# Performance work log

Hardware: AMD Instinct MI355X
Metric: run time of the kernel (lower is better)

The kernel has to match this reference:

```python
import jax, jax.numpy as jnp
import numpy as np
from jax import lax

B, T, S, H, E, V = 32, 64, 64, 512, 512, 32000


def setup_inputs() -> dict:
    key = jax.random.key(0)
    ks = jax.random.split(key, 10)
    s = 0.02
    return {
        "sequence": jax.random.randint(ks[0], (B, T), 0, V),
        "encoder_outputs": jax.random.normal(ks[1], (S, B, H), jnp.float32),
        "encoder_hidden": jax.random.normal(ks[2], (B, H), jnp.float32),
        "encoder_cell": jax.random.normal(ks[3], (B, H), jnp.float32),
        "embedding": jax.random.normal(ks[4], (V, E), jnp.float32) * s,
        "W_ih": jax.random.normal(ks[5], (4 * H, E + H), jnp.float32) * s,
        "b_ih": jnp.zeros((4 * H,), jnp.float32),
        "W_hh": jax.random.normal(ks[6], (4 * H, H), jnp.float32) * s,
        "b_hh": jnp.zeros((4 * H,), jnp.float32),
        "W_in_proj": jax.random.normal(ks[7], (H, H), jnp.float32) * s,
        "b_in_proj": jnp.zeros((H,), jnp.float32),
        "W_out_proj": jax.random.normal(ks[8], (H, 2 * H), jnp.float32) * s,
        "b_out_proj": jnp.zeros((H,), jnp.float32),
        "W_final": jax.random.normal(ks[9], (V, H), jnp.float32) * s,
        "b_final": jnp.zeros((V,), jnp.float32),
    }


def reference(sequence, encoder_outputs, encoder_hidden, encoder_cell,
              embedding, W_ih, b_ih, W_hh, b_hh,
              W_in_proj, b_in_proj, W_out_proj, b_out_proj,
              W_final, b_final):
    # embed: [B,T,E] -> [T,B,E] (dropout_in = 0 -> identity)
    x = embedding[sequence].transpose(1, 0, 2)
    input_feed = jnp.zeros((B, H), x.dtype)

    def step(carry, x_t):
        h, c, feed = carry
        inp = jnp.concatenate([x_t, feed], axis=1)          # [B, E+H]
        gates = inp @ W_ih.T + b_ih + h @ W_hh.T + b_hh     # [B, 4H]
        i, f, g, o = jnp.split(gates, 4, axis=1)
        c = jax.nn.sigmoid(f) * c + jax.nn.sigmoid(i) * jnp.tanh(g)
        h = jax.nn.sigmoid(o) * jnp.tanh(c)
        # attention layer (scores computed but unused downstream, as in source)
        xp = h @ W_in_proj.T + b_in_proj                    # [B, H]
        scores = jax.nn.softmax(
            jnp.einsum('sbh,bh->sb', encoder_outputs, xp), axis=0)  # [S, B]
        out = jnp.tanh(jnp.concatenate([xp, h], axis=1) @ W_out_proj.T + b_out_proj)
        return (h, c, out), (out, scores)

    _, (outs, _attn) = lax.scan(step, (encoder_hidden, encoder_cell, input_feed), x)
    # outs: [T,B,H] -> [B,T,H] -> logits [B,T,V]
    logits = outs.transpose(1, 0, 2) @ W_final.T + b_final
    return logits
```

## Files before the change

### kernel.cpp

```cpp
#include <hip/hip_runtime.h>
#include <hip/hip_bf16.h>

#define BB 32
#define TT 64
#define HH 512
#define EE 512
#define VV 32000

typedef float f32x4 __attribute__((ext_vector_type(4)));
typedef float f32x16 __attribute__((ext_vector_type(16)));
typedef __bf16 bf16x8 __attribute__((ext_vector_type(8)));
typedef unsigned short u16x8 __attribute__((ext_vector_type(8)));

static __device__ __forceinline__ unsigned short f2bf(float f) {
  unsigned int u = __builtin_bit_cast(unsigned int, f);
  u += 0x7fffu + ((u >> 16) & 1u);
  return (unsigned short)(u >> 16);
}

static __device__ __forceinline__ void gload16(const void* g, void* l) {
  __builtin_amdgcn_global_load_lds(
      (const __attribute__((address_space(1))) void*)g,
      (__attribute__((address_space(3))) void*)l, 16, 0, 0);
}

__global__ __launch_bounds__(256) void k_cvt_bf16(const float* __restrict__ in,
                                                  unsigned short* __restrict__ out,
                                                  int n8) {
  int tid = blockIdx.x * 256 + threadIdx.x;
  if (tid >= n8) return;
  int idx = tid * 8;
  float4 a = *(const float4*)(in + idx);
  float4 b = *(const float4*)(in + idx + 4);
  u16x8 o;
  o[0] = f2bf(a.x); o[1] = f2bf(a.y); o[2] = f2bf(a.z); o[3] = f2bf(a.w);
  o[4] = f2bf(b.x); o[5] = f2bf(b.y); o[6] = f2bf(b.z); o[7] = f2bf(b.w);
  *(u16x8*)(out + idx) = o;
}

__global__ __launch_bounds__(256) void k_trcvt(const float* __restrict__ in,
                                               unsigned short* __restrict__ out) {
  __shared__ float tile[32][33];
  const int tx = threadIdx.x & 31, ty = threadIdx.x >> 5;
  const int k0 = blockIdx.x * 32, m0 = blockIdx.y * 32;
#pragma unroll
  for (int r = 0; r < 4; ++r)
    tile[ty + r * 8][tx] = in[(size_t)(k0 + ty + r * 8) * 512 + m0 + tx];
  __syncthreads();
#pragma unroll
  for (int r = 0; r < 4; ++r)
    out[(size_t)(m0 + ty + r * 8) * 512 + k0 + tx] = f2bf(tile[tx][ty + r * 8]);
}

__global__ __launch_bounds__(256) void k_emb(const int* __restrict__ seq,
                                             const float* __restrict__ emb,
                                             unsigned short* __restrict__ out) {
  int tid = blockIdx.x * 256 + threadIdx.x;
  int idx = tid * 8;
  int m = idx >> 9;
  int e0 = idx & 511;
  int t = m >> 5, b = m & 31;
  int s = seq[b * TT + t];
  const float* src = emb + (size_t)s * EE + e0;
  float4 a = *(const float4*)(src);
  float4 c = *(const float4*)(src + 4);
  u16x8 o;
  o[0] = f2bf(a.x); o[1] = f2bf(a.y); o[2] = f2bf(a.z); o[3] = f2bf(a.w);
  o[4] = f2bf(c.x); o[5] = f2bf(c.y); o[6] = f2bf(c.z); o[7] = f2bf(c.w);
  *(u16x8*)(out + m * EE + e0) = o;
}

__global__ __launch_bounds__(256) void k_beff(const float* __restrict__ W_out,
                                              const float* __restrict__ b_in,
                                              const float* __restrict__ b_out,
                                              float* __restrict__ b_eff) {
  int i = blockIdx.x * 256 + threadIdx.x;
  if (i >= HH) return;
  float acc = b_out[i];
  for (int k = 0; k < HH; ++k) acc += W_out[i * 1024 + k] * b_in[k];
  b_eff[i] = acc;
}

__global__ __launch_bounds__(256) void k_gemm(const unsigned short* __restrict__ A, int lda,
                                              const unsigned short* __restrict__ Bm, int ldb,
                                              float* __restrict__ C, int ldc,
                                              const float* __restrict__ bias1,
                                              const float* __restrict__ bias2,
                                              const float* __restrict__ biasR1,
                                              const float* __restrict__ biasR2,
                                              const float* __restrict__ Cadd, int ldadd,
                                              int K, int m_panels) {
  __shared__ unsigned short As[128 * 32];
  __shared__ unsigned short Bs[128 * 32];
  const int tx = threadIdx.x;
  const int lane = tx & 63, w = tx >> 6;
  const int wrow = (w >> 1) * 64, wcol = (w & 1) * 64;
  const int l15 = lane & 15, lk = lane >> 4;
  const int nb = gridDim.x;
  const int swz = (blockIdx.x & 7) * (nb >> 3) + (blockIdx.x >> 3);
  const int m0 = (swz % m_panels) * 128, n0 = (swz / m_panels) * 128;
  const int r_lane = lane >> 2;
  const int k_lane = (lane & 3) * 8;
  f32x4 acc[4][4] = {};
  for (int k0 = 0; k0 < K; k0 += 32) {
#pragma unroll
    for (int h = 0; h < 2; ++h) {
      int r0 = w * 32 + h * 16;
      gload16(A + (size_t)(m0 + r0 + r_lane) * lda + k0 + k_lane, &As[r0 * 32]);
      gload16(Bm + (size_t)(n0 + r0 + r_lane) * ldb + k0 + k_lane, &Bs[r0 * 32]);
    }
    asm volatile("s_waitcnt vmcnt(0)" ::: "memory");
    __syncthreads();
    bf16x8 av[4], bv[4];
#pragma unroll
    for (int mi = 0; mi < 4; ++mi)
      av[mi] = __builtin_bit_cast(bf16x8, *(const int4*)(&As[(wrow + mi * 16 + l15) * 32 + lk * 8]));
#pragma unroll
    for (int ni = 0; ni < 4; ++ni)
      bv[ni] = __builtin_bit_cast(bf16x8, *(const int4*)(&Bs[(wcol + ni * 16 + l15) * 32 + lk * 8]));
#pragma unroll
    for (int mi = 0; mi < 4; ++mi)
#pragma unroll
      for (int ni = 0; ni < 4; ++ni)
        acc[mi][ni] = __builtin_amdgcn_mfma_f32_16x16x32_bf16(av[mi], bv[ni], acc[mi][ni], 0, 0, 0);
    __syncthreads();
  }
#pragma unroll
  for (int mi = 0; mi < 4; ++mi) {
#pragma unroll
    for (int ni = 0; ni < 4; ++ni) {
      int row = m0 + wrow + mi * 16 + lk * 4;
      int col = n0 + wcol + ni * 16 + l15;
      float bb = 0.f;
      if (bias1) bb += bias1[col];
      if (bias2) bb += bias2[col];
#pragma unroll
      for (int q = 0; q < 4; ++q) {
        float bR = 0.f;
        if (biasR1) bR += biasR1[row + q];
        if (biasR2) bR += biasR2[row + q];
        float ad = Cadd ? Cadd[(size_t)(row + q) * ldadd + col] : 0.f;
        C[(size_t)(row + q) * ldc + col] = acc[mi][ni][q] + bb + bR + ad;
      }
    }
  }
}

static __device__ __forceinline__ void gbar(unsigned* __restrict__ bar, unsigned gen) {
  __syncthreads();
  if (threadIdx.x == 0) {
    asm volatile("s_waitcnt vmcnt(0)" ::: "memory");
    __hip_atomic_store(&bar[blockIdx.x], gen, __ATOMIC_RELAXED, __HIP_MEMORY_SCOPE_AGENT);
  }
  if (threadIdx.x < 64) {
    while (__hip_atomic_load(&bar[threadIdx.x], __ATOMIC_RELAXED, __HIP_MEMORY_SCOPE_AGENT) < gen) {}
  }
  __syncthreads();
  asm volatile("" ::: "memory");
}

__global__ __launch_bounds__(256, 1) void k_recur(
    const float* __restrict__ xprojT,
    const unsigned short* __restrict__ wih_b,
    const unsigned short* __restrict__ whh_b,
    const unsigned short* __restrict__ weff_b,
    const float* __restrict__ b_eff,
    const float* __restrict__ enc_c,
    unsigned short* __restrict__ h_ext,
    unsigned short* __restrict__ outs_ext,
    unsigned* __restrict__ bar)
{
  __shared__ int4 Abuf4[4096];
  __shared__ float red[4][32][32];
  char* Abuf = (char*)Abuf4;

  const int tx = threadIdx.x;
  const int bid = blockIdx.x;
  const int i0 = bid * 8;
  const int w = tx >> 6, l = tx & 63;
  const int jl = l & 31;
  const int kh = (l >> 5) * 8;
  const int u = tx >> 5, b = tx & 31;

  bf16x8 wg[16];
  {
    const int jg = (jl >> 3) * 512 + i0 + (jl & 7);
#pragma unroll
    for (int r = 0; r < 16; ++r) {
      int k0 = (w * 16 + r) * 16 + kh;
      const unsigned short* src = (k0 < 512)
          ? wih_b + (size_t)jg * 1024 + 512 + k0
          : whh_b + (size_t)jg * 512 + (k0 - 512);
      wg[r] = __builtin_bit_cast(bf16x8, *(const int4*)src);
    }
  }
  bf16x8 we[8];
  {
    const int wr = (bid >> 2) * 32 + jl;
#pragma unroll
    for (int r = 0; r < 8; ++r) {
      int k0 = (w * 8 + r) * 16 + kh;
      we[r] = __builtin_bit_cast(bf16x8, *(const int4*)(weff_b + (size_t)wr * 512 + k0));
    }
  }
  float c_reg = enc_c[b * 512 + i0 + u];
  const float be = b_eff[i0 + u];

  auto stage = [&](const unsigned short* __restrict__ src, int half) {
#pragma unroll
    for (int rnd = 0; rnd < 8; ++rnd) {
      int id = rnd * 256 + tx;
      int row = id >> 6, c16 = id & 63;
      int4 v = *(const int4*)(src + (size_t)row * 512 + c16 * 8);
      int byte = (row * 2048 + half * 1024 + c16 * 16) ^ ((row & 7) << 4);
      *(int4*)(Abuf + byte) = v;
    }
  };
  auto afrag = [&](int ktile) -> bf16x8 {
    int byte = (jl * 2048 + ktile * 32 + (l >> 5) * 16) ^ ((jl & 7) << 4);
    return __builtin_bit_cast(bf16x8, *(const int4*)(Abuf + byte));
  };

  stage(outs_ext, 0);
  stage(h_ext, 1);
  __syncthreads();

  unsigned gen = 1;
  for (int t = 0; t < 64; ++t) {
    float xp[4];
#pragma unroll
    for (int g = 0; g < 4; ++g)
      xp[g] = xprojT[(size_t)(g * 512 + i0 + u) * 2048 + t * 32 + b];
    f32x16 acc = {};
#pragma unroll
    for (int r = 0; r < 16; ++r)
      acc = __builtin_amdgcn_mfma_f32_32x32x16_bf16(wg[r], afrag(w * 16 + r), acc, 0, 0, 0);
#pragma unroll
    for (int reg = 0; reg < 16; ++reg) {
      int row = (reg & 3) + 8 * (reg >> 2) + 4 * (l >> 5);
      red[w][row][jl] = acc[reg];
    }
    __syncthreads();
    {
      float g4[4];
#pragma unroll
      for (int g = 0; g < 4; ++g)
        g4[g] = red[0][g * 8 + u][b] + red[1][g * 8 + u][b]
              + red[2][g * 8 + u][b] + red[3][g * 8 + u][b] + xp[g];
      float si = 1.f / (1.f + __expf(-g4[0]));
      float sf = 1.f / (1.f + __expf(-g4[1]));
      float so = 1.f / (1.f + __expf(-g4[3]));
      float cn = sf * c_reg + si * tanhf(g4[2]);
      c_reg = cn;
      unsigned hb = f2bf(so * tanhf(cn));
      unsigned other = (unsigned)__shfl_down((int)hb, 32);
      if ((u & 1) == 0) {
        unsigned* h32 = (unsigned*)(h_ext + (size_t)(t + 1) * 16384);
        __hip_atomic_store(&h32[b * 256 + bid * 4 + (u >> 1)], hb | (other << 16),
                           __ATOMIC_RELAXED, __HIP_MEMORY_SCOPE_AGENT);
      }
    }
    gbar(bar, gen++);

    stage(h_ext + (size_t)(t + 1) * 16384, 1);
    __syncthreads();
    f32x16 acc2 = {};
#pragma unroll
    for (int r = 0; r < 8; ++r)
      acc2 = __builtin_amdgcn_mfma_f32_32x32x16_bf16(we[r], afrag(32 + w * 8 + r), acc2, 0, 0, 0);
#pragma unroll
    for (int reg = 0; reg < 16; ++reg) {
      int row = (reg & 3) + 8 * (reg >> 2) + 4 * (l >> 5);
      red[w][row][jl] = acc2[reg];
    }
    __syncthreads();
    {
      int row = (bid & 3) * 8 + u;
      float s = red[0][row][b] + red[1][row][b] + red[2][row][b] + red[3][row][b] + be;
      unsigned ob = f2bf(tanhf(s));
      unsigned other = (unsigned)__shfl_down((int)ob, 32);
      if ((u & 1) == 0) {
        unsigned* o32 = (unsigned*)(outs_ext + (size_t)(t + 1) * 16384);
        __hip_atomic_store(&o32[b * 256 + bid * 4 + (u >> 1)], ob | (other << 16),
                           __ATOMIC_RELAXED, __HIP_MEMORY_SCOPE_AGENT);
      }
    }
    gbar(bar, gen++);

    if (t < 63) {
      stage(outs_ext + (size_t)(t + 1) * 16384, 0);
      __syncthreads();
    }
  }
}

__global__ __launch_bounds__(256) void k_tr(const unsigned short* __restrict__ outs,
                                            unsigned short* __restrict__ abt) {
  int tid = blockIdx.x * 256 + threadIdx.x;
  int idx = tid * 8;
  int m = idx >> 9;
  int h0 = idx & 511;
  int b = m >> 6, t = m & 63;
  *(u16x8*)(abt + m * 512 + h0) =
      *(const u16x8*)(outs + (size_t)(t * 32 + b) * 512 + h0);
}

extern "C" void kernel_launch(void* const* d_in, const int* in_sizes, int n_in,
                              void* d_out, int out_size, void* d_ws, size_t ws_size,
                              hipStream_t stream) {
  const int*   seq      = (const int*)d_in[0];
  const float* enc_h    = (const float*)d_in[2];
  const float* enc_c    = (const float*)d_in[3];
  const float* emb      = (const float*)d_in[4];
  const float* W_ih     = (const float*)d_in[5];
  const float* b_ih     = (const float*)d_in[6];
  const float* W_hh     = (const float*)d_in[7];
  const float* b_hh     = (const float*)d_in[8];
  const float* W_inp    = (const float*)d_in[9];
  const float* b_inp    = (const float*)d_in[10];
  const float* W_outp   = (const float*)d_in[11];
  const float* b_outp   = (const float*)d_in[12];
  const float* W_final  = (const float*)d_in[13];
  const float* b_final  = (const float*)d_in[14];
  float* logits = (float*)d_out;

  char* ws = (char*)d_ws;
  size_t off = 0;
  auto alloc = [&](size_t bytes) {
    char* p = ws + off;
    off += (bytes + 255) & ~(size_t)255;
    return p;
  };
  unsigned short* wih_b  = (unsigned short*)alloc((size_t)2048 * 1024 * 2);
  unsigned short* whh_b  = (unsigned short*)alloc((size_t)2048 * 512 * 2);
  unsigned short* wfin_b = (unsigned short*)alloc((size_t)VV * HH * 2);
  unsigned short* weff_b = (unsigned short*)alloc((size_t)512 * 512 * 2);
  unsigned short* wout_b = (unsigned short*)alloc((size_t)512 * 1024 * 2);
  unsigned short* win_t  = (unsigned short*)alloc((size_t)512 * 512 * 2);
  unsigned short* emb_b  = (unsigned short*)alloc((size_t)2048 * 512 * 2);
  float* xprojT = (float*)alloc((size_t)2048 * 2048 * 4);
  float* W_eff  = (float*)alloc((size_t)512 * 512 * 4);
  float* b_eff  = (float*)alloc((size_t)512 * 4);
  unsigned short* h_ext  = (unsigned short*)alloc((size_t)65 * 32 * 512 * 2);
  unsigned short* outs_e = (unsigned short*)alloc((size_t)65 * 32 * 512 * 2);
  unsigned short* abt = (unsigned short*)alloc((size_t)2048 * 512 * 2);
  unsigned* bar = (unsigned*)alloc(4096);

  hipMemsetAsync(bar, 0, 4096, stream);
  hipMemsetAsync(outs_e, 0, (size_t)32 * 512 * 2, stream);

  hipLaunchKernelGGL(k_cvt_bf16, dim3(1024), dim3(256), 0, stream, W_ih, wih_b, 2048 * 1024 / 8);
  hipLaunchKernelGGL(k_cvt_bf16, dim3(512), dim3(256), 0, stream, W_hh, whh_b, 2048 * 512 / 8);
  hipLaunchKernelGGL(k_cvt_bf16, dim3(8000), dim3(256), 0, stream, W_final, wfin_b, VV * HH / 8);
  hipLaunchKernelGGL(k_cvt_bf16, dim3(8), dim3(256), 0, stream, enc_h, h_ext, 32 * 512 / 8);
  hipLaunchKernelGGL(k_cvt_bf16, dim3(256), dim3(256), 0, stream, W_outp, wout_b, 512 * 1024 / 8);
  hipLaunchKernelGGL(k_trcvt, dim3(16, 16), dim3(256), 0, stream, W_inp, win_t);
  hipLaunchKernelGGL(k_emb, dim3(512), dim3(256), 0, stream, seq, emb, emb_b);
  hipLaunchKernelGGL(k_beff, dim3(2), dim3(256), 0, stream, W_outp, b_inp, b_outp, b_eff);

  hipLaunchKernelGGL(k_gemm, dim3(16), dim3(256), 0, stream,
                     wout_b, 1024, win_t, 512, W_eff, 512,
                     (const float*)nullptr, (const float*)nullptr,
                     (const float*)nullptr, (const float*)nullptr,
                     W_outp + 512, 1024, 512, 4);
  hipLaunchKernelGGL(k_cvt_bf16, dim3(128), dim3(256), 0, stream, W_eff, weff_b, 512 * 512 / 8);

  hipLaunchKernelGGL(k_gemm, dim3(256), dim3(256), 0, stream,
                     wih_b, 1024, emb_b, 512, xprojT, 2048,
                     (const float*)nullptr, (const float*)nullptr, b_ih, b_hh,
                     (const float*)nullptr, 0, 512, 16);

  hipLaunchKernelGGL(k_recur, dim3(64), dim3(256), 0, stream,
                     xprojT, wih_b, whh_b, weff_b, b_eff, enc_c,
                     h_ext, outs_e, bar);

  hipLaunchKernelGGL(k_tr, dim3(512), dim3(256), 0, stream, outs_e + 16384, abt);
  hipLaunchKernelGGL(k_gemm, dim3(4000), dim3(256), 0, stream,
                     abt, 512, wfin_b, 512, logits, 32000,
                     b_final, (const float*)nullptr, (const float*)nullptr, (const float*)nullptr,
                     (const float*)nullptr, 0, 512, 16);
}
```

Before: 834.8 us.

## Specialize final vocab GEMM with larger tiles, swizzled grid and nontemporal stores

Replaces the generic GEMM for the final logits projection with a dedicated kernel using 256x128 tiles and XOR-swizzled LDS layout. Blocks are remapped so those sharing B tiles run together, and the fp32 logits are written with nontemporal stores. The grid-barrier spin loop also gains an s_sleep to reduce polling pressure. Larger tiles raise register use and reduce the number of blocks, and there is no double buffering, so load latency is not hidden.

```diff
diff --git a/kernel.cpp b/kernel.cpp
--- a/kernel.cpp
+++ b/kernel.cpp
@@ -146,6 +146,78 @@
   }
 }
 
+__global__ __launch_bounds__(256) void k_gemm2(const unsigned short* __restrict__ A,
+                                               const unsigned short* __restrict__ Bm,
+                                               float* __restrict__ C,
+                                               const float* __restrict__ biasN) {
+  __shared__ unsigned short As[256 * 64];
+  __shared__ unsigned short Bs[128 * 64];
+  const int tx = threadIdx.x;
+  const int lane = tx & 63, w = tx >> 6;
+  const int wrow = (w >> 1) * 128, wcol = (w & 1) * 64;
+  const int l15 = lane & 15, lk = lane >> 4;
+  const int nb = gridDim.x;
+  const int swz = (blockIdx.x & 7) * (nb >> 3) + (blockIdx.x >> 3);
+  const int m0 = (swz & 7) * 256, n0 = (swz >> 3) * 128;
+  const int lr = lane >> 3, lc = lane & 7;
+  f32x4 acc[8][4] = {};
+  for (int k0 = 0; k0 < 512; k0 += 64) {
+#pragma unroll
+    for (int i = 0; i < 8; ++i) {
+      int row = w * 64 + i * 8 + lr;
+      int csw = lc ^ (row & 7);
+      gload16(A + (size_t)(m0 + row) * 512 + k0 + csw * 8, &As[(w * 64 + i * 8) * 64]);
+    }
+#pragma unroll
+    for (int i = 0; i < 4; ++i) {
+      int row = w * 32 + i * 8 + lr;
+      int csw = lc ^ (row & 7);
+      gload16(Bm + (size_t)(n0 + row) * 512 + k0 + csw * 8, &Bs[(w * 32 + i * 8) * 64]);
+    }
+    asm volatile("s_waitcnt vmcnt(0)" ::: "memory");
+    __syncthreads();
+#pragma unroll
+    for (int kk = 0; kk < 2; ++kk) {
+      bf16x8 av[8], bv[4];
+      const char* Ab = (const char*)As;
+      const char* Bb = (const char*)Bs;
+#pragma unroll
+      for (int mi = 0; mi < 8; ++mi) {
+        int row = wrow + mi * 16 + l15;
+        int c = kk * 4 + lk;
+        av[mi] = __builtin_bit_cast(bf16x8,
+            *(const int4*)(Ab + row * 128 + ((c ^ (row & 7)) << 4)));
+      }
+#pragma unroll
+      for (int ni = 0; ni < 4; ++ni) {
+        int row = wcol + ni * 16 + l15;
+        int c = kk * 4 + lk;
+        bv[ni] = __builtin_bit_cast(bf16x8,
+            *(const int4*)(Bb + row * 128 + ((c ^ (row & 7)) << 4)));
+      }
+#pragma unroll
+      for (int mi = 0; mi < 8; ++mi)
+#pragma unroll
+        for (int ni = 0; ni < 4; ++ni)
+          acc[mi][ni] = __builtin_amdgcn_mfma_f32_16x16x32_bf16(av[mi], bv[ni], acc[mi][ni], 0, 0, 0);
+    }
+    __syncthreads();
+  }
+#pragma unroll
+  for (int mi = 0; mi < 8; ++mi) {
+#pragma unroll
+    for (int ni = 0; ni < 4; ++ni) {
+      int row = m0 + wrow + mi * 16 + lk * 4;
+      int col = n0 + wcol + ni * 16 + l15;
+      float bb = biasN[col];
+#pragma unroll
+      for (int q = 0; q < 4; ++q)
+        __builtin_nontemporal_store(acc[mi][ni][q] + bb,
+                                    &C[(size_t)(row + q) * 32000 + col]);
+    }
+  }
+}
+
 static __device__ __forceinline__ void gbar(unsigned* __restrict__ bar, unsigned gen) {
   __syncthreads();
   if (threadIdx.x == 0) {
@@ -153,7 +225,8 @@
     __hip_atomic_store(&bar[blockIdx.x], gen, __ATOMIC_RELAXED, __HIP_MEMORY_SCOPE_AGENT);
   }
   if (threadIdx.x < 64) {
-    while (__hip_atomic_load(&bar[threadIdx.x], __ATOMIC_RELAXED, __HIP_MEMORY_SCOPE_AGENT) < gen) {}
+    while (__hip_atomic_load(&bar[threadIdx.x], __ATOMIC_RELAXED, __HIP_MEMORY_SCOPE_AGENT) < gen)
+      __builtin_amdgcn_s_sleep(1);
   }
   __syncthreads();
   asm volatile("" ::: "memory");
@@ -375,8 +448,6 @@
                      h_ext, outs_e, bar);
 
   hipLaunchKernelGGL(k_tr, dim3(512), dim3(256), 0, stream, outs_e + 16384, abt);
-  hipLaunchKernelGGL(k_gemm, dim3(4000), dim3(256), 0, stream,
-                     abt, 512, wfin_b, 512, logits, 32000,
-                     b_final, (const float*)nullptr, (const float*)nullptr, (const float*)nullptr,
-                     (const float*)nullptr, 0, 512, 16);
-}
+  hipLaunchKernelGGL(k_gemm2, dim3(2000), dim3(256), 0, stream,
+                     abt, wfin_b, logits, b_final);
+}
```

After: 797.0 us. 1.05x faster.
